# Performance work log

Measured on AMD Instinct MI355X. Metric: run time of the kernel, lower is better.

The kernel has to match this reference:

```python
import jax, jax.numpy as jnp
import numpy as np

D = 512
HEAD_NUMB = 8

def setup_inputs() -> dict:
    key = jax.random.key(0)
    k1, k2, k3 = jax.random.split(key, 3)
    x = jax.random.normal(k1, (4, 4096, D), dtype=jnp.float32)
    # nn.Linear(D, 3D): weight [3D, D], bias [3D]
    W_qkv = jax.random.normal(k2, (3 * D, D), dtype=jnp.float32) / np.sqrt(D)
    b_qkv = jax.random.normal(k3, (3 * D,), dtype=jnp.float32) * 0.01
    return {"x": x, "W_qkv": W_qkv, "b_qkv": b_qkv}

def reference(x, W_qkv, b_qkv):
    # fused QKV projection: x @ W^T + b  -> [B, N, 3D]
    qkv = jnp.einsum('bnd,ed->bne', x, W_qkv) + b_qkv
    q = qkv[:, :, :D]
    k = qkv[:, :, D:2 * D]
    v = qkv[:, :, 2 * D:]
    scaling = (D / HEAD_NUMB) ** (-0.5)
    # single-head attention over full D (faithful to the original module)
    scores = jnp.einsum('bqd,bkd->bqk', q, k) * scaling  # [B, N, N]
    attn = jax.nn.softmax(scores, axis=2)
    return jnp.einsum('bqk,bkd->bqd', attn, v)
```

## Files before the change

kernel.cpp:

```cpp
#include <hip/hip_runtime.h>
#include <hip/hip_bf16.h>

#define D_DIM 512
#define NSEQ  4096
#define BATCH 4
#define SCALE 0.125f

typedef __attribute__((ext_vector_type(8)))  short short8;
typedef __attribute__((ext_vector_type(16))) float floatx16;

__device__ __forceinline__ unsigned short f2bf(float f) {
    __hip_bfloat16 h = __float2bfloat16(f);
    return *reinterpret_cast<unsigned short*>(&h);
}

__device__ __forceinline__ floatx16 mfma_bf16(short8 a, short8 b, floatx16 c) {
    return __builtin_amdgcn_mfma_f32_32x32x16_bf16(a, b, c, 0, 0, 0);
}

#define GLOAD16(g, l) __builtin_amdgcn_global_load_lds( \
    (const __attribute__((address_space(1))) unsigned int*)(g), \
    (__attribute__((address_space(3))) unsigned int*)(l), 16, 0, 0)

__global__ __launch_bounds__(256) void cast_inputs(
    const float* __restrict__ x, const float* __restrict__ W,
    unsigned short* __restrict__ xb, unsigned short* __restrict__ Wb)
{
    const size_t NX = (size_t)BATCH * NSEQ * D_DIM;
    size_t i = ((size_t)blockIdx.x * 256 + threadIdx.x) * 8;
    const float* src; unsigned short* dst;
    if (i < NX) { src = x + i; dst = xb + i; }
    else        { src = W + (i - NX); dst = Wb + (i - NX); }
    float4 v0 = *(const float4*)(src);
    float4 v1 = *(const float4*)(src + 4);
    short8 h;
    h[0] = (short)f2bf(v0.x); h[1] = (short)f2bf(v0.y);
    h[2] = (short)f2bf(v0.z); h[3] = (short)f2bf(v0.w);
    h[4] = (short)f2bf(v1.x); h[5] = (short)f2bf(v1.y);
    h[6] = (short)f2bf(v1.z); h[7] = (short)f2bf(v1.w);
    *(short8*)dst = h;
}

__global__ __launch_bounds__(256, 2) void qkv_gemm(
    const unsigned short* __restrict__ xb, const unsigned short* __restrict__ Wb,
    const float* __restrict__ bias,
    unsigned short* __restrict__ qs, unsigned short* __restrict__ kk,
    unsigned short* __restrict__ vT)
{
    __shared__ __align__(16) unsigned short Xs[128 * 64];
    __shared__ __align__(16) unsigned short Ws[128 * 64];

    const int t = threadIdx.x;
    const int lane = t & 63, w = t >> 6;
    const int l31 = lane & 31, lh = lane >> 5;
    const int wm = w >> 1, we = w & 1;
    const int m0 = blockIdx.x * 128;
    const int n0 = blockIdx.y * 128;

    floatx16 a00, a01, a10, a11;
#pragma unroll
    for (int r = 0; r < 16; r++) { a00[r] = 0.f; a01[r] = 0.f; a10[r] = 0.f; a11[r] = 0.f; }

    int rowp[4], colp[4];
#pragma unroll
    for (int p = 0; p < 4; p++) {
        int o = p * 4096 + t * 16;
        int row = o >> 7;
        int sl  = ((o >> 4) & 7) ^ (row & 7);
        rowp[p] = row; colp[p] = sl * 8;
    }

    for (int kc = 0; kc < 8; kc++) {
        const int k0 = kc * 64;
        __syncthreads();
#pragma unroll
        for (int p = 0; p < 4; p++) {
            GLOAD16(xb + (size_t)(m0 + rowp[p]) * D_DIM + k0 + colp[p],
                    (char*)Xs + p * 4096 + (t & ~63) * 16);
            GLOAD16(Wb + (size_t)(n0 + rowp[p]) * D_DIM + k0 + colp[p],
                    (char*)Ws + p * 4096 + (t & ~63) * 16);
        }
        __syncthreads();
        const int sw = l31 & 7;
#pragma unroll
        for (int ks = 0; ks < 4; ks++) {
            const int s = ks * 2 + lh;
            const int cof = ((s ^ sw) * 8);
            short8 fa0 = *(const short8*)&Xs[(wm * 64 +      l31) * 64 + cof];
            short8 fa1 = *(const short8*)&Xs[(wm * 64 + 32 + l31) * 64 + cof];
            short8 fb0 = *(const short8*)&Ws[(we * 64 +      l31) * 64 + cof];
            short8 fb1 = *(const short8*)&Ws[(we * 64 + 32 + l31) * 64 + cof];
            a00 = mfma_bf16(fa0, fb0, a00);
            a01 = mfma_bf16(fa0, fb1, a01);
            a10 = mfma_bf16(fa1, fb0, a10);
            a11 = mfma_bf16(fa1, fb1, a11);
        }
    }

#pragma unroll
    for (int jt = 0; jt < 2; jt++) {
        const int e = n0 + we * 64 + jt * 32 + l31;
        const float bv = bias[e];
#pragma unroll
        for (int it = 0; it < 2; it++) {
            const int mb = m0 + wm * 64 + it * 32;
            const floatx16& av = (it == 0) ? ((jt == 0) ? a00 : a01)
                                           : ((jt == 0) ? a10 : a11);
            if (e < 512) {
#pragma unroll
                for (int r = 0; r < 16; r++) {
                    int m = mb + (r & 3) + 8 * (r >> 2) + 4 * lh;
                    qs[(size_t)m * D_DIM + e] = f2bf((av[r] + bv) * SCALE);
                }
            } else if (e < 1024) {
#pragma unroll
                for (int r = 0; r < 16; r++) {
                    int m = mb + (r & 3) + 8 * (r >> 2) + 4 * lh;
                    kk[(size_t)m * D_DIM + (e - 512)] = f2bf(av[r] + bv);
                }
            } else {
                const int d = e - 1024;
#pragma unroll
                for (int q = 0; q < 4; q++) {
                    int mq = mb + 8 * q + 4 * lh;
                    int bb = mq >> 12; int tok = mq & 4095;
                    ushort4 hv;
                    hv.x = f2bf(av[4 * q + 0] + bv); hv.y = f2bf(av[4 * q + 1] + bv);
                    hv.z = f2bf(av[4 * q + 2] + bv); hv.w = f2bf(av[4 * q + 3] + bv);
                    *(ushort4*)&vT[((size_t)bb * 512 + d) * 4096 + tok] = hv;
                }
            }
        }
    }
}

#define FA_BQ 64
#define FA_BK 256
#define FA_DC 128
#define QC_STR 136
#define KC_STR 136
#define P_STR  264
#define VT_STR 72

__global__ __launch_bounds__(512, 2) void flash_attn(
    const unsigned short* __restrict__ qs, const unsigned short* __restrict__ kk,
    const unsigned short* __restrict__ vT, float* __restrict__ out)
{
    __shared__ __align__(16) unsigned char smem[123392];
    unsigned short* Qc = (unsigned short*)(smem);
    unsigned short* Kc = (unsigned short*)(smem + 17408);
    unsigned short* Vt = (unsigned short*)(smem);
    unsigned short* P  = (unsigned short*)(smem + 87040);
    float* pmax    = (float*)(smem + 120832);
    float* psum    = (float*)(smem + 121856);
    float* alpha_s = (float*)(smem + 122880);
    float* l_s     = (float*)(smem + 123136);

    const int t = threadIdx.x;
    const int lane = t & 63, w = t >> 6;
    const int l31 = lane & 31, lh = lane >> 5;
    const int wi = w & 1, wjj = w >> 1;
    const int b  = blockIdx.y;
    const int q0 = blockIdx.x * FA_BQ;
    const size_t qbase = ((size_t)b * NSEQ + q0) * D_DIM;
    const size_t kbase = (size_t)b * NSEQ * D_DIM;
    const size_t vbase = (size_t)b * D_DIM * NSEQ;

    const int i_my = wi * 32 + l31;

    floatx16 o00, o01, o10, o11;
#pragma unroll
    for (int r = 0; r < 16; r++) { o00[r] = 0.f; o01[r] = 0.f; o10[r] = 0.f; o11[r] = 0.f; }
    float m_st = -__builtin_inff(), l_st = 0.f;

    for (int kt = 0; kt < NSEQ; kt += FA_BK) {
        floatx16 s0, s1;
#pragma unroll
        for (int r = 0; r < 16; r++) { s0[r] = 0.f; s1[r] = 0.f; }

        for (int dc = 0; dc < D_DIM; dc += FA_DC) {
            __syncthreads();
#pragma unroll
            for (int p = 0; p < 2; p++) {
                int id = t + p * 512;
                int row = id >> 4, c8 = id & 15;
                uint4 v = *(const uint4*)(qs + qbase + (size_t)row * D_DIM + dc + c8 * 8);
                *(uint4*)&Qc[row * QC_STR + c8 * 8] = v;
            }
#pragma unroll
            for (int p = 0; p < 8; p++) {
                int id = t + p * 512;
                int row = id >> 4, c8 = id & 15;
                uint4 v = *(const uint4*)(kk + kbase + (size_t)(kt + row) * D_DIM + dc + c8 * 8);
                *(uint4*)&Kc[row * KC_STR + c8 * 8] = v;
            }
            __syncthreads();
            const unsigned short* kr0 = &Kc[(wjj * 64 + l31) * KC_STR];
            const unsigned short* kr1 = kr0 + 32 * KC_STR;
            const unsigned short* qr  = &Qc[i_my * QC_STR];
#pragma unroll
            for (int ks = 0; ks < 8; ks++) {
                const int co = ks * 16 + lh * 8;
                short8 fa0 = *(const short8*)(kr0 + co);
                short8 fa1 = *(const short8*)(kr1 + co);
                short8 fb  = *(const short8*)(qr + co);
                s0 = mfma_bf16(fa0, fb, s0);
                s1 = mfma_bf16(fa1, fb, s1);
            }
        }

        float mx = -__builtin_inff();
#pragma unroll
        for (int r = 0; r < 16; r++) mx = fmaxf(mx, fmaxf(s0[r], s1[r]));
        mx = fmaxf(mx, __shfl_xor(mx, 32));
        if (lh == 0) pmax[i_my * 4 + wjj] = mx;
        __syncthreads();
        float4 pm = *(float4*)&pmax[i_my * 4];
        const float m_new = fmaxf(m_st, fmaxf(fmaxf(pm.x, pm.y), fmaxf(pm.z, pm.w)));
        const float alpha = __expf(m_st - m_new);
        m_st = m_new;

        float sum = 0.f;
        {
            const int prow = i_my * P_STR;
#pragma unroll
            for (int q = 0; q < 4; q++) {
                float p0 = __expf(s0[4*q+0] - m_new), p1 = __expf(s0[4*q+1] - m_new);
                float p2 = __expf(s0[4*q+2] - m_new), p3 = __expf(s0[4*q+3] - m_new);
                sum += (p0 + p1) + (p2 + p3);
                ushort4 h; h.x = f2bf(p0); h.y = f2bf(p1); h.z = f2bf(p2); h.w = f2bf(p3);
                *(ushort4*)&P[prow + (wjj*2+0)*32 + 8*q + 4*lh] = h;
            }
#pragma unroll
            for (int q = 0; q < 4; q++) {
                float p0 = __expf(s1[4*q+0] - m_new), p1 = __expf(s1[4*q+1] - m_new);
                float p2 = __expf(s1[4*q+2] - m_new), p3 = __expf(s1[4*q+3] - m_new);
                sum += (p0 + p1) + (p2 + p3);
                ushort4 h; h.x = f2bf(p0); h.y = f2bf(p1); h.z = f2bf(p2); h.w = f2bf(p3);
                *(ushort4*)&P[prow + (wjj*2+1)*32 + 8*q + 4*lh] = h;
            }
        }
        sum += __shfl_xor(sum, 32);
        if (lh == 0) psum[i_my * 4 + wjj] = sum;
        if (lh == 0 && wjj == 0) alpha_s[i_my] = alpha;
        __syncthreads();
        float4 ps = *(float4*)&psum[i_my * 4];
        l_st = l_st * alpha + ((ps.x + ps.y) + (ps.z + ps.w));

        float av[2][16];
        bool ch = false;
#pragma unroll
        for (int it = 0; it < 2; it++)
#pragma unroll
            for (int q = 0; q < 4; q++) {
                float4 a4 = *(float4*)&alpha_s[it * 32 + 8 * q + 4 * lh];
                av[it][4*q+0] = a4.x; av[it][4*q+1] = a4.y;
                av[it][4*q+2] = a4.z; av[it][4*q+3] = a4.w;
                ch = ch || (a4.x != 1.f) || (a4.y != 1.f) || (a4.z != 1.f) || (a4.w != 1.f);
            }
        if (__any(ch)) {
#pragma unroll
            for (int r = 0; r < 16; r++) {
                o00[r] *= av[0][r]; o01[r] *= av[0][r];
                o10[r] *= av[1][r]; o11[r] *= av[1][r];
            }
        }

        for (int jc = 0; jc < 4; jc++) {
            __syncthreads();
#pragma unroll
            for (int p = 0; p < 8; p++) {
                int id = t + p * 512;
                int d = id >> 3, c8 = id & 7;
                uint4 v = *(const uint4*)(vT + vbase + (size_t)d * NSEQ + kt + jc * 64 + c8 * 8);
                *(uint4*)&Vt[d * VT_STR + c8 * 8] = v;
            }
            __syncthreads();
            const unsigned short* pr0 = &P[l31 * P_STR + jc * 64];
            const unsigned short* pr1 = &P[(32 + l31) * P_STR + jc * 64];
            const unsigned short* vr0 = &Vt[(w * 64 + l31) * VT_STR];
            const unsigned short* vr1 = vr0 + 32 * VT_STR;
#pragma unroll
            for (int js = 0; js < 4; js++) {
                const int co = js * 16 + lh * 8;
                short8 pa0 = *(const short8*)(pr0 + co);
                short8 pa1 = *(const short8*)(pr1 + co);
                short8 vb0 = *(const short8*)(vr0 + co);
                short8 vb1 = *(const short8*)(vr1 + co);
                o00 = mfma_bf16(pa0, vb0, o00);
                o01 = mfma_bf16(pa0, vb1, o01);
                o10 = mfma_bf16(pa1, vb0, o10);
                o11 = mfma_bf16(pa1, vb1, o11);
            }
        }
    }

    if (lh == 0 && wjj == 0) l_s[i_my] = l_st;
    __syncthreads();
    float iv[2][16];
#pragma unroll
    for (int it = 0; it < 2; it++)
#pragma unroll
        for (int q = 0; q < 4; q++) {
            float4 l4 = *(float4*)&l_s[it * 32 + 8 * q + 4 * lh];
            iv[it][4*q+0] = 1.f / l4.x; iv[it][4*q+1] = 1.f / l4.y;
            iv[it][4*q+2] = 1.f / l4.z; iv[it][4*q+3] = 1.f / l4.w;
        }
#pragma unroll
    for (int it = 0; it < 2; it++) {
        const floatx16& oa = (it == 0) ? o00 : o10;
        const floatx16& ob = (it == 0) ? o01 : o11;
#pragma unroll
        for (int r = 0; r < 16; r++) {
            const int i = it * 32 + (r & 3) + 8 * (r >> 2) + 4 * lh;
            const size_t rowb = ((size_t)b * NSEQ + q0 + i) * D_DIM;
            out[rowb + w * 64 + l31]      = oa[r] * iv[it][r];
            out[rowb + w * 64 + 32 + l31] = ob[r] * iv[it][r];
        }
    }
}

extern "C" void kernel_launch(void* const* d_in, const int* in_sizes, int n_in,
                              void* d_out, int out_size, void* d_ws, size_t ws_size,
                              hipStream_t stream)
{
    (void)in_sizes; (void)n_in; (void)out_size; (void)ws_size;
    const float* x    = (const float*)d_in[0];
    const float* W    = (const float*)d_in[1];
    const float* bias = (const float*)d_in[2];
    float* out = (float*)d_out;

    unsigned short* qs = (unsigned short*)d_ws;
    unsigned short* kk = qs + (size_t)16384 * 512;
    unsigned short* vT = kk + (size_t)16384 * 512;
    unsigned short* xb = vT + (size_t)BATCH * D_DIM * NSEQ;
    unsigned short* Wb = xb + (size_t)16384 * 512;

    cast_inputs<<<dim3(4480), 256, 0, stream>>>(x, W, xb, Wb);
    qkv_gemm<<<dim3(128, 12), 256, 0, stream>>>(xb, Wb, bias, qs, kk, vT);
    flash_attn<<<dim3(NSEQ / FA_BQ, BATCH), 512, 0, stream>>>(qs, kk, vT, out);
}
```

Measured before the change: 341.9 us.

## Register-prefetch next tiles in attention and stage V transpose through LDS

In the attention kernel, the global loads for the next Q/K chunk or V chunk are issued into registers right after the barrier. They are written to LDS at the next step, so memory latency overlaps the MFMA work, and the MFMA loops run at raised wave priority. The QKV GEMM swaps grid axes so blocks sharing an x-tile run adjacently. The V output is transposed through a swizzled LDS buffer so that vT gets coalesced 16-byte stores instead of scattered 8-byte ones. This adds register pressure in the attention kernel, which could lower occupancy, plus an extra barrier in the GEMM epilogue.

After: 734.1 us. +114.7%, slower.

```diff
diff --git a/kernel.cpp b/kernel.cpp
--- a/kernel.cpp
+++ b/kernel.cpp
@@ -47,15 +47,17 @@
     unsigned short* __restrict__ qs, unsigned short* __restrict__ kk,
     unsigned short* __restrict__ vT)
 {
-    __shared__ __align__(16) unsigned short Xs[128 * 64];
-    __shared__ __align__(16) unsigned short Ws[128 * 64];
+    __shared__ __align__(16) unsigned short S2[2][128 * 64];
+    unsigned short* Xs = S2[0];
+    unsigned short* Ws = S2[1];
+    unsigned short* Tr = &S2[0][0];
 
     const int t = threadIdx.x;
     const int lane = t & 63, w = t >> 6;
     const int l31 = lane & 31, lh = lane >> 5;
     const int wm = w >> 1, we = w & 1;
-    const int m0 = blockIdx.x * 128;
-    const int n0 = blockIdx.y * 128;
+    const int n0 = blockIdx.x * 128;
+    const int m0 = blockIdx.y * 128;
 
     floatx16 a00, a01, a10, a11;
 #pragma unroll
@@ -97,39 +99,63 @@
         }
     }
 
-#pragma unroll
-    for (int jt = 0; jt < 2; jt++) {
-        const int e = n0 + we * 64 + jt * 32 + l31;
-        const float bv = bias[e];
-#pragma unroll
-        for (int it = 0; it < 2; it++) {
-            const int mb = m0 + wm * 64 + it * 32;
-            const floatx16& av = (it == 0) ? ((jt == 0) ? a00 : a01)
-                                           : ((jt == 0) ? a10 : a11);
-            if (e < 512) {
-#pragma unroll
-                for (int r = 0; r < 16; r++) {
-                    int m = mb + (r & 3) + 8 * (r >> 2) + 4 * lh;
-                    qs[(size_t)m * D_DIM + e] = f2bf((av[r] + bv) * SCALE);
+    if (n0 < 1024) {
+#pragma unroll
+        for (int jt = 0; jt < 2; jt++) {
+            const int e = n0 + we * 64 + jt * 32 + l31;
+            const float bv = bias[e];
+#pragma unroll
+            for (int it = 0; it < 2; it++) {
+                const int mb = m0 + wm * 64 + it * 32;
+                const floatx16& av = (it == 0) ? ((jt == 0) ? a00 : a01)
+                                               : ((jt == 0) ? a10 : a11);
+                if (e < 512) {
+#pragma unroll
+                    for (int r = 0; r < 16; r++) {
+                        int m = mb + (r & 3) + 8 * (r >> 2) + 4 * lh;
+                        qs[(size_t)m * D_DIM + e] = f2bf((av[r] + bv) * SCALE);
+                    }
+                } else {
+#pragma unroll
+                    for (int r = 0; r < 16; r++) {
+                        int m = mb + (r & 3) + 8 * (r >> 2) + 4 * lh;
+                        kk[(size_t)m * D_DIM + (e - 512)] = f2bf(av[r] + bv);
+                    }
                 }
-            } else if (e < 1024) {
-#pragma unroll
-                for (int r = 0; r < 16; r++) {
-                    int m = mb + (r & 3) + 8 * (r >> 2) + 4 * lh;
-                    kk[(size_t)m * D_DIM + (e - 512)] = f2bf(av[r] + bv);
-                }
-            } else {
-                const int d = e - 1024;
+            }
+        }
+    } else {
+        __syncthreads();
+#pragma unroll
+        for (int jt = 0; jt < 2; jt++) {
+            const int dd = we * 64 + jt * 32 + l31;
+            const float bv = bias[n0 + dd];
+#pragma unroll
+            for (int it = 0; it < 2; it++) {
+                const floatx16& av = (it == 0) ? ((jt == 0) ? a00 : a01)
+                                               : ((jt == 0) ? a10 : a11);
 #pragma unroll
                 for (int q = 0; q < 4; q++) {
-                    int mq = mb + 8 * q + 4 * lh;
-                    int bb = mq >> 12; int tok = mq & 4095;
+                    int tt = wm * 64 + it * 32 + 8 * q + 4 * lh;
                     ushort4 hv;
                     hv.x = f2bf(av[4 * q + 0] + bv); hv.y = f2bf(av[4 * q + 1] + bv);
                     hv.z = f2bf(av[4 * q + 2] + bv); hv.w = f2bf(av[4 * q + 3] + bv);
-                    *(ushort4*)&vT[((size_t)bb * 512 + d) * 4096 + tok] = hv;
+                    int byte = dd * 256 + ((((tt >> 3) ^ (dd & 7)) << 4)) + ((tt & 7) << 1);
+                    *(ushort4*)((char*)Tr + byte) = hv;
                 }
             }
+        }
+        __syncthreads();
+        const int rown = t >> 4;
+        const int c    = t & 15;
+        const int bb = m0 >> 12, tok0 = (m0 & 4095);
+#pragma unroll
+        for (int g = 0; g < 8; g++) {
+            int row = g * 16 + rown;
+            int byte = row * 256 + ((c ^ (row & 7)) << 4);
+            uint4 v = *(const uint4*)((char*)Tr + byte);
+            *(uint4*)(vT + ((size_t)bb * 512 + (n0 - 1024) + row) * 4096
+                      + tok0 + c * 8) = v;
         }
     }
 }
@@ -168,36 +194,65 @@
 
     const int i_my = wi * 32 + l31;
 
+    const int gqk0 = (t >> 4) * D_DIM + (t & 15) * 8;
+    const int gv0  = (t >> 3) * NSEQ  + (t & 7) * 8;
+    const int lqk0 = (t >> 4) * QC_STR + (t & 15) * 8;
+    const int lv0  = (t >> 3) * VT_STR + (t & 7) * 8;
+
+    uint4 rq[2], rk[8];
+
+#define ISSUE_QK(kt_, dc_) do {                                               \
+    _Pragma("unroll")                                                         \
+    for (int p = 0; p < 2; p++)                                               \
+        rq[p] = *(const uint4*)(qs + qbase + gqk0 + p * 32 * D_DIM + (dc_));  \
+    _Pragma("unroll")                                                         \
+    for (int p = 0; p < 8; p++)                                               \
+        rk[p] = *(const uint4*)(kk + kbase + gqk0 + p * 32 * D_DIM            \
+                                + (size_t)(kt_) * D_DIM + (dc_));             \
+} while (0)
+
+#define ISSUE_V(kt_, jc_) do {                                                \
+    _Pragma("unroll")                                                         \
+    for (int p = 0; p < 8; p++)                                               \
+        rk[p] = *(const uint4*)(vT + vbase + gv0 + p * 64 * NSEQ              \
+                                + (kt_) + (jc_) * 64);                        \
+} while (0)
+
+#define WRITE_QK() do {                                                       \
+    _Pragma("unroll")                                                         \
+    for (int p = 0; p < 2; p++) *(uint4*)&Qc[lqk0 + p * 32 * QC_STR] = rq[p]; \
+    _Pragma("unroll")                                                         \
+    for (int p = 0; p < 8; p++) *(uint4*)&Kc[lqk0 + p * 32 * KC_STR] = rk[p]; \
+} while (0)
+
+#define WRITE_V() do {                                                        \
+    _Pragma("unroll")                                                         \
+    for (int p = 0; p < 8; p++) *(uint4*)&Vt[lv0 + p * 64 * VT_STR] = rk[p];  \
+} while (0)
+
     floatx16 o00, o01, o10, o11;
 #pragma unroll
     for (int r = 0; r < 16; r++) { o00[r] = 0.f; o01[r] = 0.f; o10[r] = 0.f; o11[r] = 0.f; }
     float m_st = -__builtin_inff(), l_st = 0.f;
 
+    ISSUE_QK(0, 0);
+
     for (int kt = 0; kt < NSEQ; kt += FA_BK) {
         floatx16 s0, s1;
 #pragma unroll
         for (int r = 0; r < 16; r++) { s0[r] = 0.f; s1[r] = 0.f; }
 
+#pragma unroll
         for (int dc = 0; dc < D_DIM; dc += FA_DC) {
             __syncthreads();
-#pragma unroll
-            for (int p = 0; p < 2; p++) {
-                int id = t + p * 512;
-                int row = id >> 4, c8 = id & 15;
-                uint4 v = *(const uint4*)(qs + qbase + (size_t)row * D_DIM + dc + c8 * 8);
-                *(uint4*)&Qc[row * QC_STR + c8 * 8] = v;
-            }
-#pragma unroll
-            for (int p = 0; p < 8; p++) {
-                int id = t + p * 512;
-                int row = id >> 4, c8 = id & 15;
-                uint4 v = *(const uint4*)(kk + kbase + (size_t)(kt + row) * D_DIM + dc + c8 * 8);
-                *(uint4*)&Kc[row * KC_STR + c8 * 8] = v;
-            }
+            WRITE_QK();
             __syncthreads();
+            if (dc + FA_DC < D_DIM) ISSUE_QK(kt, dc + FA_DC);
+            else                    ISSUE_V(kt, 0);
             const unsigned short* kr0 = &Kc[(wjj * 64 + l31) * KC_STR];
             const unsigned short* kr1 = kr0 + 32 * KC_STR;
             const unsigned short* qr  = &Qc[i_my * QC_STR];
+            __builtin_amdgcn_s_setprio(1);
 #pragma unroll
             for (int ks = 0; ks < 8; ks++) {
                 const int co = ks * 16 + lh * 8;
@@ -207,6 +262,7 @@
                 s0 = mfma_bf16(fa0, fb, s0);
                 s1 = mfma_bf16(fa1, fb, s1);
             }
+            __builtin_amdgcn_s_setprio(0);
         }
 
         float mx = -__builtin_inff();
@@ -266,20 +322,18 @@
             }
         }
 
+#pragma unroll
         for (int jc = 0; jc < 4; jc++) {
             __syncthreads();
-#pragma unroll
-            for (int p = 0; p < 8; p++) {
-                int id = t + p * 512;
-                int d = id >> 3, c8 = id & 7;
-                uint4 v = *(const uint4*)(vT + vbase + (size_t)d * NSEQ + kt + jc * 64 + c8 * 8);
-                *(uint4*)&Vt[d * VT_STR + c8 * 8] = v;
-            }
+            WRITE_V();
             __syncthreads();
+            if (jc < 3) ISSUE_V(kt, jc + 1);
+            else        ISSUE_QK((kt + FA_BK < NSEQ) ? kt + FA_BK : kt, 0);
             const unsigned short* pr0 = &P[l31 * P_STR + jc * 64];
             const unsigned short* pr1 = &P[(32 + l31) * P_STR + jc * 64];
             const unsigned short* vr0 = &Vt[(w * 64 + l31) * VT_STR];
             const unsigned short* vr1 = vr0 + 32 * VT_STR;
+            __builtin_amdgcn_s_setprio(1);
 #pragma unroll
             for (int js = 0; js < 4; js++) {
                 const int co = js * 16 + lh * 8;
@@ -292,6 +346,7 @@
                 o10 = mfma_bf16(pa1, vb0, o10);
                 o11 = mfma_bf16(pa1, vb1, o11);
             }
+            __builtin_amdgcn_s_setprio(0);
         }
     }
 
@@ -318,6 +373,10 @@
             out[rowb + w * 64 + 32 + l31] = ob[r] * iv[it][r];
         }
     }
+#undef ISSUE_QK
+#undef ISSUE_V
+#undef WRITE_QK
+#undef WRITE_V
 }
 
 extern "C" void kernel_launch(void* const* d_in, const int* in_sizes, int n_in,
@@ -337,6 +396,6 @@
     unsigned short* Wb = xb + (size_t)16384 * 512;
 
     cast_inputs<<<dim3(4480), 256, 0, stream>>>(x, W, xb, Wb);
-    qkv_gemm<<<dim3(128, 12), 256, 0, stream>>>(xb, Wb, bias, qs, kk, vT);
+    qkv_gemm<<<dim3(12, 128), 256, 0, stream>>>(xb, Wb, bias, qs, kk, vT);
     flash_attn<<<dim3(NSEQ / FA_BQ, BATCH), 512, 0, stream>>>(qs, kk, vT, out);
 }
```

## Shrink flash-attention tiles to 32 queries, 128 keys with 4 waves per block

Applied to the files above, without the earlier changes.

Restructures the flash attention kernel to use a 32-row query tile, 128-key tile and 256 threads (4 waves), with each wave owning a 32-key slice for QK^T and a 128-wide output slice for PV. Shared memory drops from about 123KB to about 53KB and the grid doubles, aiming for more resident blocks and better occupancy. It also adds s_setprio around MFMA loops. The trade-off is that K and V tiles are reloaded twice as often per query, which raises global and LDS traffic per unit of work.

New measurement: 709.7 us. +107.6%, slower.

```diff
diff --git a/kernel.cpp b/kernel.cpp
--- a/kernel.cpp
+++ b/kernel.cpp
@@ -134,86 +134,84 @@
     }
 }
 
-#define FA_BQ 64
-#define FA_BK 256
+#define FA_BQ 32
+#define FA_BK 128
 #define FA_DC 128
 #define QC_STR 136
 #define KC_STR 136
-#define P_STR  264
-#define VT_STR 72
-
-__global__ __launch_bounds__(512, 2) void flash_attn(
+#define P_STR  136
+#define VT_STR 36
+
+__global__ __launch_bounds__(256, 2) void flash_attn(
     const unsigned short* __restrict__ qs, const unsigned short* __restrict__ kk,
     const unsigned short* __restrict__ vT, float* __restrict__ out)
 {
-    __shared__ __align__(16) unsigned char smem[123392];
+    __shared__ __align__(16) unsigned char smem[53504];
     unsigned short* Qc = (unsigned short*)(smem);
-    unsigned short* Kc = (unsigned short*)(smem + 17408);
+    unsigned short* Kc = (unsigned short*)(smem + 8704);
     unsigned short* Vt = (unsigned short*)(smem);
-    unsigned short* P  = (unsigned short*)(smem + 87040);
-    float* pmax    = (float*)(smem + 120832);
-    float* psum    = (float*)(smem + 121856);
-    float* alpha_s = (float*)(smem + 122880);
-    float* l_s     = (float*)(smem + 123136);
+    unsigned short* P  = (unsigned short*)(smem + 43520);
+    float* pmax    = (float*)(smem + 52224);
+    float* psum    = (float*)(smem + 52736);
+    float* alpha_s = (float*)(smem + 53248);
+    float* l_s     = (float*)(smem + 53376);
 
     const int t = threadIdx.x;
     const int lane = t & 63, w = t >> 6;
     const int l31 = lane & 31, lh = lane >> 5;
-    const int wi = w & 1, wjj = w >> 1;
     const int b  = blockIdx.y;
     const int q0 = blockIdx.x * FA_BQ;
     const size_t qbase = ((size_t)b * NSEQ + q0) * D_DIM;
     const size_t kbase = (size_t)b * NSEQ * D_DIM;
     const size_t vbase = (size_t)b * D_DIM * NSEQ;
 
-    const int i_my = wi * 32 + l31;
-
-    floatx16 o00, o01, o10, o11;
-#pragma unroll
-    for (int r = 0; r < 16; r++) { o00[r] = 0.f; o01[r] = 0.f; o10[r] = 0.f; o11[r] = 0.f; }
+    const int i_my = l31;
+
+    floatx16 o0, o1, o2, o3;
+#pragma unroll
+    for (int r = 0; r < 16; r++) { o0[r] = 0.f; o1[r] = 0.f; o2[r] = 0.f; o3[r] = 0.f; }
     float m_st = -__builtin_inff(), l_st = 0.f;
 
     for (int kt = 0; kt < NSEQ; kt += FA_BK) {
-        floatx16 s0, s1;
-#pragma unroll
-        for (int r = 0; r < 16; r++) { s0[r] = 0.f; s1[r] = 0.f; }
+        floatx16 s;
+#pragma unroll
+        for (int r = 0; r < 16; r++) s[r] = 0.f;
 
         for (int dc = 0; dc < D_DIM; dc += FA_DC) {
             __syncthreads();
 #pragma unroll
             for (int p = 0; p < 2; p++) {
-                int id = t + p * 512;
+                int id = t + p * 256;
                 int row = id >> 4, c8 = id & 15;
                 uint4 v = *(const uint4*)(qs + qbase + (size_t)row * D_DIM + dc + c8 * 8);
                 *(uint4*)&Qc[row * QC_STR + c8 * 8] = v;
             }
 #pragma unroll
             for (int p = 0; p < 8; p++) {
-                int id = t + p * 512;
+                int id = t + p * 256;
                 int row = id >> 4, c8 = id & 15;
                 uint4 v = *(const uint4*)(kk + kbase + (size_t)(kt + row) * D_DIM + dc + c8 * 8);
                 *(uint4*)&Kc[row * KC_STR + c8 * 8] = v;
             }
             __syncthreads();
-            const unsigned short* kr0 = &Kc[(wjj * 64 + l31) * KC_STR];
-            const unsigned short* kr1 = kr0 + 32 * KC_STR;
-            const unsigned short* qr  = &Qc[i_my * QC_STR];
+            const unsigned short* kr = &Kc[(w * 32 + l31) * KC_STR];
+            const unsigned short* qr = &Qc[i_my * QC_STR];
+            __builtin_amdgcn_s_setprio(1);
 #pragma unroll
             for (int ks = 0; ks < 8; ks++) {
                 const int co = ks * 16 + lh * 8;
-                short8 fa0 = *(const short8*)(kr0 + co);
-                short8 fa1 = *(const short8*)(kr1 + co);
-                short8 fb  = *(const short8*)(qr + co);
-                s0 = mfma_bf16(fa0, fb, s0);
-                s1 = mfma_bf16(fa1, fb, s1);
-            }
+                short8 fa = *(const short8*)(kr + co);
+                short8 fb = *(const short8*)(qr + co);
+                s = mfma_bf16(fa, fb, s);
+            }
+            __builtin_amdgcn_s_setprio(0);
         }
 
         float mx = -__builtin_inff();
 #pragma unroll
-        for (int r = 0; r < 16; r++) mx = fmaxf(mx, fmaxf(s0[r], s1[r]));
+        for (int r = 0; r < 16; r++) mx = fmaxf(mx, s[r]);
         mx = fmaxf(mx, __shfl_xor(mx, 32));
-        if (lh == 0) pmax[i_my * 4 + wjj] = mx;
+        if (lh == 0) pmax[i_my * 4 + w] = mx;
         __syncthreads();
         float4 pm = *(float4*)&pmax[i_my * 4];
         const float m_new = fmaxf(m_st, fmaxf(fmaxf(pm.x, pm.y), fmaxf(pm.z, pm.w)));
@@ -225,97 +223,80 @@
             const int prow = i_my * P_STR;
 #pragma unroll
             for (int q = 0; q < 4; q++) {
-                float p0 = __expf(s0[4*q+0] - m_new), p1 = __expf(s0[4*q+1] - m_new);
-                float p2 = __expf(s0[4*q+2] - m_new), p3 = __expf(s0[4*q+3] - m_new);
+                float p0 = __expf(s[4*q+0] - m_new), p1 = __expf(s[4*q+1] - m_new);
+                float p2 = __expf(s[4*q+2] - m_new), p3 = __expf(s[4*q+3] - m_new);
                 sum += (p0 + p1) + (p2 + p3);
                 ushort4 h; h.x = f2bf(p0); h.y = f2bf(p1); h.z = f2bf(p2); h.w = f2bf(p3);
-                *(ushort4*)&P[prow + (wjj*2+0)*32 + 8*q + 4*lh] = h;
-            }
-#pragma unroll
-            for (int q = 0; q < 4; q++) {
-                float p0 = __expf(s1[4*q+0] - m_new), p1 = __expf(s1[4*q+1] - m_new);
-                float p2 = __expf(s1[4*q+2] - m_new), p3 = __expf(s1[4*q+3] - m_new);
-                sum += (p0 + p1) + (p2 + p3);
-                ushort4 h; h.x = f2bf(p0); h.y = f2bf(p1); h.z = f2bf(p2); h.w = f2bf(p3);
-                *(ushort4*)&P[prow + (wjj*2+1)*32 + 8*q + 4*lh] = h;
+                *(ushort4*)&P[prow + w * 32 + 8 * q + 4 * lh] = h;
             }
         }
         sum += __shfl_xor(sum, 32);
-        if (lh == 0) psum[i_my * 4 + wjj] = sum;
-        if (lh == 0 && wjj == 0) alpha_s[i_my] = alpha;
+        if (lh == 0) psum[i_my * 4 + w] = sum;
+        if (lh == 0 && w == 0) alpha_s[i_my] = alpha;
         __syncthreads();
         float4 ps = *(float4*)&psum[i_my * 4];
         l_st = l_st * alpha + ((ps.x + ps.y) + (ps.z + ps.w));
 
-        float av[2][16];
+        float av[16];
         bool ch = false;
 #pragma unroll
-        for (int it = 0; it < 2; it++)
-#pragma unroll
-            for (int q = 0; q < 4; q++) {
-                float4 a4 = *(float4*)&alpha_s[it * 32 + 8 * q + 4 * lh];
-                av[it][4*q+0] = a4.x; av[it][4*q+1] = a4.y;
-                av[it][4*q+2] = a4.z; av[it][4*q+3] = a4.w;
-                ch = ch || (a4.x != 1.f) || (a4.y != 1.f) || (a4.z != 1.f) || (a4.w != 1.f);
-            }
+        for (int q = 0; q < 4; q++) {
+            float4 a4 = *(float4*)&alpha_s[8 * q + 4 * lh];
+            av[4*q+0] = a4.x; av[4*q+1] = a4.y; av[4*q+2] = a4.z; av[4*q+3] = a4.w;
+            ch = ch || (a4.x != 1.f) || (a4.y != 1.f) || (a4.z != 1.f) || (a4.w != 1.f);
+        }
         if (__any(ch)) {
 #pragma unroll
             for (int r = 0; r < 16; r++) {
-                o00[r] *= av[0][r]; o01[r] *= av[0][r];
-                o10[r] *= av[1][r]; o11[r] *= av[1][r];
+                o0[r] *= av[r]; o1[r] *= av[r]; o2[r] *= av[r]; o3[r] *= av[r];
             }
         }
 
         for (int jc = 0; jc < 4; jc++) {
+            if (jc > 0) __syncthreads();
+#pragma unroll
+            for (int p = 0; p < 8; p++) {
+                int id = t + p * 256;
+                int d = id >> 2, c = id & 3;
+                uint4 v = *(const uint4*)(vT + vbase + (size_t)d * NSEQ + kt + jc * 32 + c * 8);
+                *(uint4*)&Vt[d * VT_STR + c * 8] = v;
+            }
             __syncthreads();
-#pragma unroll
-            for (int p = 0; p < 8; p++) {
-                int id = t + p * 512;
-                int d = id >> 3, c8 = id & 7;
-                uint4 v = *(const uint4*)(vT + vbase + (size_t)d * NSEQ + kt + jc * 64 + c8 * 8);
-                *(uint4*)&Vt[d * VT_STR + c8 * 8] = v;
-            }
-            __syncthreads();
-            const unsigned short* pr0 = &P[l31 * P_STR + jc * 64];
-            const unsigned short* pr1 = &P[(32 + l31) * P_STR + jc * 64];
-            const unsigned short* vr0 = &Vt[(w * 64 + l31) * VT_STR];
-            const unsigned short* vr1 = vr0 + 32 * VT_STR;
-#pragma unroll
-            for (int js = 0; js < 4; js++) {
-                const int co = js * 16 + lh * 8;
-                short8 pa0 = *(const short8*)(pr0 + co);
-                short8 pa1 = *(const short8*)(pr1 + co);
-                short8 vb0 = *(const short8*)(vr0 + co);
-                short8 vb1 = *(const short8*)(vr1 + co);
-                o00 = mfma_bf16(pa0, vb0, o00);
-                o01 = mfma_bf16(pa0, vb1, o01);
-                o10 = mfma_bf16(pa1, vb0, o10);
-                o11 = mfma_bf16(pa1, vb1, o11);
-            }
-        }
-    }
-
-    if (lh == 0 && wjj == 0) l_s[i_my] = l_st;
+            const unsigned short* pr = &P[l31 * P_STR + jc * 32];
+            __builtin_amdgcn_s_setprio(1);
+#pragma unroll
+            for (int dt = 0; dt < 4; dt++) {
+                const unsigned short* vr = &Vt[(w * 128 + dt * 32 + l31) * VT_STR];
+                floatx16& od = (dt == 0) ? o0 : (dt == 1) ? o1 : (dt == 2) ? o2 : o3;
+#pragma unroll
+                for (int js = 0; js < 2; js++) {
+                    const int co = js * 16 + lh * 8;
+                    short8 pa = *(const short8*)(pr + co);
+                    short8 vb = *(const short8*)(vr + co);
+                    od = mfma_bf16(pa, vb, od);
+                }
+            }
+            __builtin_amdgcn_s_setprio(0);
+        }
+    }
+
+    if (lh == 0 && w == 0) l_s[i_my] = l_st;
     __syncthreads();
-    float iv[2][16];
-#pragma unroll
-    for (int it = 0; it < 2; it++)
-#pragma unroll
-        for (int q = 0; q < 4; q++) {
-            float4 l4 = *(float4*)&l_s[it * 32 + 8 * q + 4 * lh];
-            iv[it][4*q+0] = 1.f / l4.x; iv[it][4*q+1] = 1.f / l4.y;
-            iv[it][4*q+2] = 1.f / l4.z; iv[it][4*q+3] = 1.f / l4.w;
-        }
-#pragma unroll
-    for (int it = 0; it < 2; it++) {
-        const floatx16& oa = (it == 0) ? o00 : o10;
-        const floatx16& ob = (it == 0) ? o01 : o11;
+    float iv[16];
+#pragma unroll
+    for (int q = 0; q < 4; q++) {
+        float4 l4 = *(float4*)&l_s[8 * q + 4 * lh];
+        iv[4*q+0] = 1.f / l4.x; iv[4*q+1] = 1.f / l4.y;
+        iv[4*q+2] = 1.f / l4.z; iv[4*q+3] = 1.f / l4.w;
+    }
+#pragma unroll
+    for (int dt = 0; dt < 4; dt++) {
+        const floatx16& od = (dt == 0) ? o0 : (dt == 1) ? o1 : (dt == 2) ? o2 : o3;
 #pragma unroll
         for (int r = 0; r < 16; r++) {
-            const int i = it * 32 + (r & 3) + 8 * (r >> 2) + 4 * lh;
-            const size_t rowb = ((size_t)b * NSEQ + q0 + i) * D_DIM;
-            out[rowb + w * 64 + l31]      = oa[r] * iv[it][r];
-            out[rowb + w * 64 + 32 + l31] = ob[r] * iv[it][r];
+            const int i = (r & 3) + 8 * (r >> 2) + 4 * lh;
+            out[((size_t)b * NSEQ + q0 + i) * D_DIM + w * 128 + dt * 32 + l31]
+                = od[r] * iv[r];
         }
     }
 }
@@ -338,5 +319,5 @@
 
     cast_inputs<<<dim3(4480), 256, 0, stream>>>(x, W, xb, Wb);
     qkv_gemm<<<dim3(128, 12), 256, 0, stream>>>(xb, Wb, bias, qs, kk, vT);
-    flash_attn<<<dim3(NSEQ / FA_BQ, BATCH), 512, 0, stream>>>(qs, kk, vT, out);
-}
+    flash_attn<<<dim3(NSEQ / FA_BQ, BATCH), 256, 0, stream>>>(qs, kk, vT, out);
+}
```
